# Kernel optimization log

Measured on AMD Instinct MI355X. Metric: run time of the kernel, lower is better.

## Reference

```python
import jax, jax.numpy as jnp
import numpy as np

DIM = 128
NUM_HEADS = 4
HEAD_DIM = DIM // NUM_HEADS
WS = 8            # window size (square)
SHIFT = 4         # shift size
SCALE = HEAD_DIM ** -0.5
WIN_AREA = WS * WS


def _rel_pos_index(wh, ww):
    coords = np.stack(np.meshgrid(np.arange(wh), np.arange(ww), indexing='ij'))  # (2,wh,ww)
    flat = coords.reshape(2, -1)
    rel = flat[:, :, None] - flat[:, None, :]          # (2,S,S)
    rel = rel.transpose(1, 2, 0).astype(np.int64)
    rel[:, :, 0] += wh - 1
    rel[:, :, 1] += ww - 1
    rel[:, :, 0] *= 2 * ww - 1
    return jnp.asarray(rel.sum(-1))                    # (S,S)

_REL_IDX = _rel_pos_index(WS, WS)


def setup_inputs() -> dict:
    key = jax.random.key(0)
    ks = jax.random.split(key, 6)
    B, C, U, V, H, W = 2, DIM, 5, 5, 64, 64
    return {
        'x': jax.random.normal(ks[0], (B, C, U, V, H, W), dtype=jnp.float32),
        'qkv_w': jax.random.normal(ks[1], (3 * DIM, DIM), dtype=jnp.float32) * 0.02,
        'qkv_b': jax.random.normal(ks[2], (3 * DIM,), dtype=jnp.float32) * 0.02,
        'proj_w': jax.random.normal(ks[3], (DIM, DIM), dtype=jnp.float32) * 0.02,
        'proj_b': jax.random.normal(ks[4], (DIM,), dtype=jnp.float32) * 0.02,
        'rpb_table': jax.random.normal(ks[5], ((2 * WS - 1) ** 2, NUM_HEADS), dtype=jnp.float32) * 0.02,
    }


def reference(x, qkv_w, qkv_b, proj_w, proj_b, proj_bias_unused=None, **_):
    # kept signature explicit below; see wrapper
    raise NotImplementedError


def reference(x, qkv_w, qkv_b, proj_w, proj_b, rpb_table):
    B, C, U, V, H, W = x.shape
    Hn, Wn = H // WS, W // WS
    S = WIN_AREA

    # cyclic shift (torch.roll with shifts (SHIFT,SHIFT) on dims (-1,-2))
    xs = jnp.roll(x, (SHIFT, SHIFT), axis=(-1, -2))

    # window partition: B C U V (Hn wv) (Wn wh) -> (B U V Hn Wn) (wv wh) C
    xw = xs.reshape(B, C, U, V, Hn, WS, Wn, WS)
    xw = xw.transpose(0, 2, 3, 4, 6, 5, 7, 1)          # B U V Hn Wn wv wh C
    xw = xw.reshape(-1, S, C)                          # (nW, S, C)

    # qkv projection (torch Linear: x @ W.T + b)
    qkv = xw @ qkv_w.T + qkv_b                         # (nW, S, 3C)
    nW = qkv.shape[0]
    qkv = qkv.reshape(nW, S, NUM_HEADS, 3 * HEAD_DIM).transpose(0, 2, 1, 3)  # (nW,h,S,3d)
    q, k, v = jnp.split(qkv, 3, axis=-1)               # each (nW,h,S,d)

    attn = jnp.einsum('bhqd,bhkd->bhqk', q * SCALE, k)  # (nW,h,S,S)
    bias = rpb_table[_REL_IDX]                          # (S,S,h)
    attn = attn + bias.transpose(2, 0, 1)[None]         # (1,h,S,S) broadcast
    attn = jax.nn.softmax(attn, axis=-1)

    out = jnp.einsum('bhqk,bhkd->bhqd', attn, v)        # (nW,h,S,d)
    out = out.transpose(0, 2, 1, 3).reshape(nW, S, C)   # merge heads
    out = out @ proj_w.T + proj_b

    # window un-partition back to B C U V H W
    out = out.reshape(B, U, V, Hn, Wn, WS, WS, C)
    out = out.transpose(0, 7, 1, 2, 3, 5, 4, 6)         # B C U V Hn wv Wn wh
    out = out.reshape(B, C, U, V, H, W)

    # reverse shift
    return jnp.roll(out, (-SHIFT, -SHIFT), axis=(-1, -2))
```

## Files before the change

### kernel.cpp

```cpp
#include <hip/hip_runtime.h>

#define NH 4
#define HD 32
#define ST 64
#define CD 128
#define IMG 102400
#define VHW 20480
#define HW_ 4096
#define SCALE_ 0.17677669529663687f

typedef __attribute__((ext_vector_type(8))) short bf16x8;
typedef __attribute__((ext_vector_type(4))) float f32x4;
typedef __attribute__((ext_vector_type(4))) int   i32x4;
typedef __attribute__((ext_vector_type(2))) int   i32x2;

__device__ __forceinline__ short f2bf(float f) {
    unsigned int u = __float_as_uint(f);
    u = (u + 0x7FFF + ((u >> 16) & 1)) >> 16;
    return (short)u;
}

__device__ __forceinline__ int cvt_pk_bf16(float lo, float hi) {
    int r;
    asm("v_cvt_pk_bf16_f32 %0, %1, %2" : "=v"(r) : "v"(lo), "v"(hi));
    return r;
}

template <int N>
__device__ __forceinline__ float row_ror(float v) {
    return __int_as_float(__builtin_amdgcn_update_dpp(
        0, __float_as_int(v), 0x120 | N, 0xF, 0xF, true));
}

__global__ void cvt_w_kernel(const float* __restrict__ qkv_w,
                             const float* __restrict__ proj_w,
                             const float* __restrict__ rpb,
                             short* __restrict__ wq,
                             short* __restrict__ wp,
                             float* __restrict__ bt) {
    int i = blockIdx.x * 256 + threadIdx.x;
    if (i < 49152) wq[i] = f2bf(qkv_w[i]);
    else if (i < 65536) wp[i - 49152] = f2bf(proj_w[i - 49152]);
    else if (i < 81920) {
        int j = i - 65536;
        int hh = j >> 12, qi = (j >> 6) & 63, ln2 = (j >> 2) & 15, nt = j & 3;
        int kcol = nt * 16 + ln2;
        int ridx = ((qi >> 3) - (kcol >> 3) + 7) * 15 + ((qi & 7) - (kcol & 7) + 7);
        bt[j] = rpb[ridx * 4 + hh];
    }
}


template <bool DB>
__global__ __launch_bounds__(256, 2)
void win_attn_mfma(const float* __restrict__ x,
                   const short* __restrict__ wq,
                   const float* __restrict__ qkv_b,
                   const short* __restrict__ wp,
                   const float* __restrict__ proj_b,
                   const float* __restrict__ bias,
                   float* __restrict__ out) {
    __shared__ __align__(16) short smem[38400];

    const int t    = threadIdx.x;
    const int h    = __builtin_amdgcn_readfirstlane(t >> 6);
    const int ln   = t & 15;
    const int quad = (t >> 4) & 3;

    const int s     = t & 15;
    const int cb    = t >> 4;
    const int gr    = s >> 1;
    const int ghalf = s & 1;
    const int srow4 = s * 4;

    const int wid = (blockIdx.x & 7) * 400 + (blockIdx.x >> 3);
    const int wn = wid & 7, hn = (wid >> 3) & 7;
    int rem = wid >> 6;
    const int v = rem % 5; rem /= 5;
    const int u = rem % 5;
    const int b = rem / 5;
    const long base = (long)b * (CD * IMG) + u * VHW + v * HW_;

    const int hh_r = (((hn << 3) + gr) - 4) & 63;
    const int ww0  = (((wn << 3) + ghalf * 4) - 4) & 63;
    const long pixrs = base + hh_r * 64 + ww0;

    const int ocol = (((wn << 3) + (quad & 1) * 4) - 4) & 63;

    short* X  = smem;
    short* Qh = smem + 8704 + h * 5120;
    short* Kh = Qh + 2560;
    short* Ph = Qh;
    short* Vh = smem + 29184 + h * 2304;
    short* O  = smem;

    float4 xv[8];
    #pragma unroll
    for (int j = 0; j < 8; ++j)
        xv[j] = *(const float4*)(x + pixrs + (long)(cb * 8 + j) * IMG);

    bf16x8 wqf[24];
    #pragma unroll
    for (int kh = 0; kh < 4; ++kh)
        #pragma unroll
        for (int n = 0; n < 6; ++n)
            wqf[kh * 6 + n] = *(const bf16x8*)(wq + (h * 96 + n * 16 + ln) * 128 + kh * 32 + quad * 8);
    float qb[6];
    #pragma unroll
    for (int n = 0; n < 6; ++n) qb[n] = qkv_b[h * 96 + n * 16 + ln];

    #pragma unroll
    for (int px = 0; px < 4; ++px) {
        i32x4 pk;
        #pragma unroll
        for (int j2 = 0; j2 < 4; ++j2)
            pk[j2] = cvt_pk_bf16(((const float*)&xv[2 * j2])[px],
                                 ((const float*)&xv[2 * j2 + 1])[px]);
        *(i32x4*)(X + (srow4 + px) * 136 + cb * 8) = pk;
    }
    __syncthreads();

    f32x4 acc[6][4];
    #pragma unroll
    for (int n = 0; n < 6; ++n)
        #pragma unroll
        for (int mt = 0; mt < 4; ++mt) acc[n][mt] = (f32x4){0.f, 0.f, 0.f, 0.f};

    #pragma unroll
    for (int kh = 0; kh < 4; ++kh) {
        bf16x8 af[4];
        #pragma unroll
        for (int mt = 0; mt < 4; ++mt)
            af[mt] = *(const bf16x8*)(X + (mt * 16 + ln) * 136 + kh * 32 + quad * 8);
        __builtin_amdgcn_s_setprio(1);
        #pragma unroll
        for (int n = 0; n < 6; ++n)
            #pragma unroll
            for (int mt = 0; mt < 4; ++mt)
                acc[n][mt] = __builtin_amdgcn_mfma_f32_16x16x32_bf16(af[mt], wqf[kh * 6 + n], acc[n][mt], 0, 0, 0);
        __builtin_amdgcn_s_setprio(0);
    }
    __syncthreads();

    #pragma unroll
    for (int n = 0; n < 4; ++n) {
        const float bv_ = qb[n];
        short* dst = (n < 2) ? Qh : Kh;
        const int col = (n & 1) * 16 + ln;
        #pragma unroll
        for (int mt = 0; mt < 4; ++mt)
            #pragma unroll
            for (int r = 0; r < 4; ++r) {
                const float val = acc[n][mt][r] + bv_;
                const int tk = mt * 16 + quad * 4 + r;
                dst[tk * 40 + col] = f2bf((n < 2) ? val * SCALE_ : val);
            }
    }
    #pragma unroll
    for (int n = 4; n < 6; ++n) {
        const float bv_ = qb[n];
        const int d = (n - 4) * 16 + ln;
        #pragma unroll
        for (int mt = 0; mt < 4; ++mt) {
            const int tk0 = mt * 16 + quad * 4;
            i32x2 pv;
            pv[0] = cvt_pk_bf16(acc[n][mt][0] + bv_, acc[n][mt][1] + bv_);
            pv[1] = cvt_pk_bf16(acc[n][mt][2] + bv_, acc[n][mt][3] + bv_);
            *(i32x2*)(Vh + d * 72 + tk0) = pv;
        }
    }

    bf16x8 aq[4], bk[4];
    #pragma unroll
    for (int mt = 0; mt < 4; ++mt) aq[mt] = *(const bf16x8*)(Qh + (mt * 16 + ln) * 40 + quad * 8);
    #pragma unroll
    for (int nt = 0; nt < 4; ++nt) bk[nt] = *(const bf16x8*)(Kh + (nt * 16 + ln) * 40 + quad * 8);

    f32x4 bb[4][4];
    if (DB) {
        const float* bt = bias + h * 4096;
        #pragma unroll
        for (int mt = 0; mt < 4; ++mt)
            #pragma unroll
            for (int r = 0; r < 4; ++r) {
                const int qi = mt * 16 + quad * 4 + r;
                bb[mt][r] = *(const f32x4*)(bt + (qi * 16 + ln) * 4);
            }
    }

    f32x4 sm[4][4];
    __builtin_amdgcn_s_setprio(1);
    #pragma unroll
    for (int mt = 0; mt < 4; ++mt)
        #pragma unroll
        for (int nt = 0; nt < 4; ++nt) {
            f32x4 z = (f32x4){0.f, 0.f, 0.f, 0.f};
            sm[mt][nt] = __builtin_amdgcn_mfma_f32_16x16x32_bf16(aq[mt], bk[nt], z, 0, 0, 0);
        }
    __builtin_amdgcn_s_setprio(0);

    if (DB) {
        #pragma unroll
        for (int mt = 0; mt < 4; ++mt)
            #pragma unroll
            for (int r = 0; r < 4; ++r)
                #pragma unroll
                for (int nt = 0; nt < 4; ++nt)
                    sm[mt][nt][r] += bb[mt][r][nt];
    } else {
        #pragma unroll
        for (int nt = 0; nt < 4; ++nt) {
            const int kcol = nt * 16 + ln;
            const int ik = kcol >> 3, jk = kcol & 7;
            #pragma unroll
            for (int mt = 0; mt < 4; ++mt)
                #pragma unroll
                for (int r = 0; r < 4; ++r) {
                    const int q = mt * 16 + quad * 4 + r;
                    const int ridx = ((q >> 3) - ik + 7) * 15 + ((q & 7) - jk + 7);
                    sm[mt][nt][r] += bias[ridx * 4 + h];
                }
        }
    }

    float inv[4][4];
    #pragma unroll
    for (int mt = 0; mt < 4; ++mt)
        #pragma unroll
        for (int r = 0; r < 4; ++r) {
            float m = fmaxf(fmaxf(sm[mt][0][r], sm[mt][1][r]), fmaxf(sm[mt][2][r], sm[mt][3][r]));
            m = fmaxf(m, row_ror<1>(m));
            m = fmaxf(m, row_ror<2>(m));
            m = fmaxf(m, row_ror<4>(m));
            m = fmaxf(m, row_ror<8>(m));
            float sum = 0.f;
            #pragma unroll
            for (int nt = 0; nt < 4; ++nt) {
                float e = __expf(sm[mt][nt][r] - m);
                sm[mt][nt][r] = e;
                sum += e;
            }
            const int q = mt * 16 + quad * 4 + r;
            #pragma unroll
            for (int nt = 0; nt < 4; ++nt)
                Ph[q * 72 + nt * 16 + ln] = f2bf(sm[mt][nt][r]);
            sum += row_ror<1>(sum);
            sum += row_ror<2>(sum);
            sum += row_ror<4>(sum);
            sum += row_ror<8>(sum);
            inv[mt][r] = 1.f / sum;
        }

    bf16x8 wpf[8];
    #pragma unroll
    for (int kt = 0; kt < 4; ++kt)
        #pragma unroll
        for (int nt = 0; nt < 2; ++nt)
            wpf[kt * 2 + nt] = *(const bf16x8*)(wp + (h * 32 + nt * 16 + ln) * 128 + kt * 32 + quad * 8);
    float pb[2];
    #pragma unroll
    for (int nt = 0; nt < 2; ++nt) pb[nt] = proj_b[h * 32 + nt * 16 + ln];

    f32x4 oa[4][2];
    #pragma unroll
    for (int mt = 0; mt < 4; ++mt)
        #pragma unroll
        for (int nt = 0; nt < 2; ++nt) oa[mt][nt] = (f32x4){0.f, 0.f, 0.f, 0.f};
    #pragma unroll
    for (int kt = 0; kt < 2; ++kt) {
        bf16x8 ap[4], bv[2];
        #pragma unroll
        for (int mt = 0; mt < 4; ++mt)
            ap[mt] = *(const bf16x8*)(Ph + (mt * 16 + ln) * 72 + kt * 32 + quad * 8);
        #pragma unroll
        for (int nt = 0; nt < 2; ++nt)
            bv[nt] = *(const bf16x8*)(Vh + (nt * 16 + ln) * 72 + kt * 32 + quad * 8);
        __builtin_amdgcn_s_setprio(1);
        #pragma unroll
        for (int mt = 0; mt < 4; ++mt)
            #pragma unroll
            for (int nt = 0; nt < 2; ++nt)
                oa[mt][nt] = __builtin_amdgcn_mfma_f32_16x16x32_bf16(ap[mt], bv[nt], oa[mt][nt], 0, 0, 0);
        __builtin_amdgcn_s_setprio(0);
    }

    #pragma unroll
    for (int mt = 0; mt < 4; ++mt)
        #pragma unroll
        for (int nt = 0; nt < 2; ++nt)
            #pragma unroll
            for (int r = 0; r < 4; ++r)
                O[(mt * 16 + quad * 4 + r) * 136 + h * 32 + nt * 16 + ln] =
                    f2bf(oa[mt][nt][r] * inv[mt][r]);
    __syncthreads();

    f32x4 pa[4][2];
    #pragma unroll
    for (int mt = 0; mt < 4; ++mt)
        #pragma unroll
        for (int nt = 0; nt < 2; ++nt) pa[mt][nt] = (f32x4){0.f, 0.f, 0.f, 0.f};
    #pragma unroll
    for (int kt = 0; kt < 4; ++kt) {
        bf16x8 ao[4];
        #pragma unroll
        for (int mt = 0; mt < 4; ++mt)
            ao[mt] = *(const bf16x8*)(O + (mt * 16 + ln) * 136 + kt * 32 + quad * 8);
        __builtin_amdgcn_s_setprio(1);
        #pragma unroll
        for (int mt = 0; mt < 4; ++mt)
            #pragma unroll
            for (int nt = 0; nt < 2; ++nt)
                pa[mt][nt] = __builtin_amdgcn_mfma_f32_16x16x32_bf16(ao[mt], wpf[kt * 2 + nt], pa[mt][nt], 0, 0, 0);
        __builtin_amdgcn_s_setprio(0);
    }

    #pragma unroll
    for (int mt = 0; mt < 4; ++mt) {
        const int orow = (((hn << 3) + 2 * mt + (quad >> 1)) - 4) & 63;
        const long prow = base + orow * 64 + ocol;
        #pragma unroll
        for (int nt = 0; nt < 2; ++nt) {
            const int c = h * 32 + nt * 16 + ln;
            f32x4 fv = pa[mt][nt] + pb[nt];
            *(f32x4*)(out + prow + (long)c * IMG) = fv;
        }
    }
}

__global__ __launch_bounds__(256, 1)
void win_attn_fallback(const float* __restrict__ x,
                       const float* __restrict__ wQKV,
                       const float* __restrict__ qkv_b,
                       const float* __restrict__ wP,
                       const float* __restrict__ proj_b,
                       const float* __restrict__ rpb,
                       float* __restrict__ out) {
    __shared__ __align__(16) float k_lds[NH * ST * HD];
    __shared__ __align__(16) float v_lds[NH * ST * HD];
    const int t = threadIdx.x;
    const int h = __builtin_amdgcn_readfirstlane(t >> 6);
    const int l = t & 63;
    const int wid = blockIdx.x;
    const int wn = wid & 7, hn = (wid >> 3) & 7;
    int rem = wid >> 6;
    const int v = rem % 5; rem /= 5;
    const int u = rem % 5;
    const int b = rem / 5;
    const int hh = (((hn << 3) + (l >> 3)) - 4) & 63;
    const int ww = (((wn << 3) + (l & 7)) - 4) & 63;
    const int pix = b * (NH * HD * IMG) + u * VHW + v * HW_ + hh * 64 + ww;
    float q[HD], kk[HD], vv[HD];
    const float* bq = qkv_b + h * 96;
    #pragma unroll
    for (int d = 0; d < HD; ++d) { q[d] = bq[d]; kk[d] = bq[32 + d]; vv[d] = bq[64 + d]; }
    for (int c = 0; c < CD; ++c) {
        float xv = x[pix + c * IMG];
        const float* wc = wQKV + h * 96 * CD + c;
        #pragma unroll
        for (int d = 0; d < HD; ++d) {
            q[d]  = fmaf(xv, wc[d * CD], q[d]);
            kk[d] = fmaf(xv, wc[(32 + d) * CD], kk[d]);
            vv[d] = fmaf(xv, wc[(64 + d) * CD], vv[d]);
        }
    }
    float* kr = k_lds + (h * ST + l) * HD;
    float* vr = v_lds + (h * ST + l) * HD;
    #pragma unroll
    for (int d = 0; d < HD; ++d) { kr[d] = kk[d]; vr[d] = vv[d]; }
    __syncthreads();
    const float* kh2 = k_lds + h * ST * HD;
    const float* vh2 = v_lds + h * ST * HD;
    const int iq = l >> 3, jq = l & 7;
    float m = -1e30f;
    for (int sk = 0; sk < ST; ++sk) {
        const float* kp = kh2 + sk * HD;
        float a2 = 0.f;
        #pragma unroll
        for (int d = 0; d < HD; ++d) a2 = fmaf(q[d], kp[d], a2);
        int ridx = (iq - (sk >> 3) + 7) * 15 + (jq - (sk & 7) + 7);
        m = fmaxf(m, fmaf(a2, SCALE_, rpb[ridx * 4 + h]));
    }
    float o[HD];
    #pragma unroll
    for (int d = 0; d < HD; ++d) o[d] = 0.f;
    float ssum = 0.f;
    for (int sk = 0; sk < ST; ++sk) {
        const float* kp = kh2 + sk * HD;
        float a2 = 0.f;
        #pragma unroll
        for (int d = 0; d < HD; ++d) a2 = fmaf(q[d], kp[d], a2);
        int ridx = (iq - (sk >> 3) + 7) * 15 + (jq - (sk & 7) + 7);
        float e = __expf(fmaf(a2, SCALE_, rpb[ridx * 4 + h]) - m);
        ssum += e;
        const float* vp = vh2 + sk * HD;
        #pragma unroll
        for (int d = 0; d < HD; ++d) o[d] = fmaf(e, vp[d], o[d]);
    }
    const float inv = 1.f / ssum;
    __syncthreads();
    float* ot = k_lds;
    #pragma unroll
    for (int d = 0; d < HD; ++d) ot[(h * HD + d) * ST + l] = o[d] * inv;
    __syncthreads();
    float o2[HD];
    const float* pb2 = proj_b + h * HD;
    #pragma unroll
    for (int j = 0; j < HD; ++j) o2[j] = pb2[j];
    for (int c = 0; c < CD; ++c) {
        float xv = ot[c * ST + l];
        const float* pc = wP + h * HD * CD + c;
        #pragma unroll
        for (int j = 0; j < HD; ++j) o2[j] = fmaf(xv, pc[j * CD], o2[j]);
    }
    float* ob = out + pix;
    #pragma unroll
    for (int j = 0; j < HD; ++j) ob[(h * HD + j) * IMG] = o2[j];
}

extern "C" void kernel_launch(void* const* d_in, const int* in_sizes, int n_in,
                              void* d_out, int out_size, void* d_ws, size_t ws_size,
                              hipStream_t stream) {
    const float* x      = (const float*)d_in[0];
    const float* qkv_w  = (const float*)d_in[1];
    const float* qkv_b  = (const float*)d_in[2];
    const float* proj_w = (const float*)d_in[3];
    const float* proj_b = (const float*)d_in[4];
    const float* rpb    = (const float*)d_in[5];
    float* out = (float*)d_out;

    const int nW = 2 * 5 * 5 * 8 * 8;
    const size_t need_w  = (size_t)(49152 + 16384) * sizeof(short);
    const size_t need_db = need_w + (size_t)16384 * sizeof(float);

    if (ws_size >= need_db) {
        short* wqs = (short*)d_ws;
        short* wps = wqs + 49152;
        float* bt  = (float*)(wqs + 65536);
        cvt_w_kernel<<<320, 256, 0, stream>>>(qkv_w, proj_w, rpb, wqs, wps, bt);
        win_attn_mfma<true><<<nW, 256, 0, stream>>>(x, wqs, qkv_b, wps, proj_b, bt, out);
    } else if (ws_size >= need_w) {
        short* wqs = (short*)d_ws;
        short* wps = wqs + 49152;
        cvt_w_kernel<<<256, 256, 0, stream>>>(qkv_w, proj_w, rpb, wqs, wps, nullptr);
        win_attn_mfma<false><<<nW, 256, 0, stream>>>(x, wqs, qkv_b, wps, proj_b, rpb, out);
    } else {
        win_attn_fallback<<<nW, 256, 0, stream>>>(x, qkv_w, qkv_b, proj_w, proj_b, rpb, out);
    }
}
```

Baseline: 272.4 us.

## Pack LDS stores via permuted head-dim layout and pre-permuted proj weights

Stores Q/K, P and the attention output to LDS as packed bf16 pairs or quads. To allow this, the head-dim columns and key columns use an interleaved order, which stays consistent because the QK^T and PV contractions are permutation-invariant over the contracted index. The proj weight columns are permuted in the conversion kernel to match the interleaved O layout. The V store changes to scalar stores in permuted token order, and an empty asm forces the wq fragment loads to be issued early. The aim is fewer LDS store instructions and bank conflicts, at the cost of tricky index consistency.

```diff
diff --git a/kernel.cpp b/kernel.cpp
--- a/kernel.cpp
+++ b/kernel.cpp
@@ -40,8 +40,12 @@
                              float* __restrict__ bt) {
     int i = blockIdx.x * 256 + threadIdx.x;
     if (i < 49152) wq[i] = f2bf(qkv_w[i]);
-    else if (i < 65536) wp[i - 49152] = f2bf(proj_w[i - 49152]);
-    else if (i < 81920) {
+    else if (i < 65536) {
+        int j = i - 49152;
+        int oc = j >> 7, cp = j & 127;
+        int src = (cp & 96) | ((cp & 1) << 4) | ((cp & 31) >> 1);
+        wp[j] = f2bf(proj_w[oc * 128 + src]);
+    } else if (i < 81920) {
         int j = i - 65536;
         int hh = j >> 12, qi = (j >> 6) & 63, ln2 = (j >> 2) & 15, nt = j & 3;
         int kcol = nt * 16 + ln2;
@@ -105,6 +109,10 @@
         #pragma unroll
         for (int n = 0; n < 6; ++n)
             wqf[kh * 6 + n] = *(const bf16x8*)(wq + (h * 96 + n * 16 + ln) * 128 + kh * 32 + quad * 8);
+    #pragma unroll
+    for (int i = 0; i < 24; ++i)
+        asm volatile("" :: "v"(wqf[i]));
+
     float qb[6];
     #pragma unroll
     for (int n = 0; n < 6; ++n) qb[n] = qkv_b[h * 96 + n * 16 + ln];
@@ -142,40 +150,6 @@
     }
     __syncthreads();
 
-    #pragma unroll
-    for (int n = 0; n < 4; ++n) {
-        const float bv_ = qb[n];
-        short* dst = (n < 2) ? Qh : Kh;
-        const int col = (n & 1) * 16 + ln;
-        #pragma unroll
-        for (int mt = 0; mt < 4; ++mt)
-            #pragma unroll
-            for (int r = 0; r < 4; ++r) {
-                const float val = acc[n][mt][r] + bv_;
-                const int tk = mt * 16 + quad * 4 + r;
-                dst[tk * 40 + col] = f2bf((n < 2) ? val * SCALE_ : val);
-            }
-    }
-    #pragma unroll
-    for (int n = 4; n < 6; ++n) {
-        const float bv_ = qb[n];
-        const int d = (n - 4) * 16 + ln;
-        #pragma unroll
-        for (int mt = 0; mt < 4; ++mt) {
-            const int tk0 = mt * 16 + quad * 4;
-            i32x2 pv;
-            pv[0] = cvt_pk_bf16(acc[n][mt][0] + bv_, acc[n][mt][1] + bv_);
-            pv[1] = cvt_pk_bf16(acc[n][mt][2] + bv_, acc[n][mt][3] + bv_);
-            *(i32x2*)(Vh + d * 72 + tk0) = pv;
-        }
-    }
-
-    bf16x8 aq[4], bk[4];
-    #pragma unroll
-    for (int mt = 0; mt < 4; ++mt) aq[mt] = *(const bf16x8*)(Qh + (mt * 16 + ln) * 40 + quad * 8);
-    #pragma unroll
-    for (int nt = 0; nt < 4; ++nt) bk[nt] = *(const bf16x8*)(Kh + (nt * 16 + ln) * 40 + quad * 8);
-
     f32x4 bb[4][4];
     if (DB) {
         const float* bt = bias + h * 4096;
@@ -187,6 +161,35 @@
                 bb[mt][r] = *(const f32x4*)(bt + (qi * 16 + ln) * 4);
             }
     }
+
+    #pragma unroll
+    for (int mt = 0; mt < 4; ++mt)
+        #pragma unroll
+        for (int r = 0; r < 4; ++r) {
+            const int tk = mt * 16 + quad * 4 + r;
+            const float q0 = (acc[0][mt][r] + qb[0]) * SCALE_;
+            const float q1 = (acc[1][mt][r] + qb[1]) * SCALE_;
+            *(int*)(Qh + tk * 40 + 2 * ln) = cvt_pk_bf16(q0, q1);
+            const float k0 = acc[2][mt][r] + qb[2];
+            const float k1 = acc[3][mt][r] + qb[3];
+            *(int*)(Kh + tk * 40 + 2 * ln) = cvt_pk_bf16(k0, k1);
+        }
+    #pragma unroll
+    for (int n = 4; n < 6; ++n) {
+        const float bv_ = qb[n];
+        const int d = (n - 4) * 16 + ln;
+        #pragma unroll
+        for (int mt = 0; mt < 4; ++mt)
+            #pragma unroll
+            for (int r = 0; r < 4; ++r)
+                Vh[d * 72 + 16 * quad + 4 * r + mt] = f2bf(acc[n][mt][r] + bv_);
+    }
+
+    bf16x8 aq[4], bk[4];
+    #pragma unroll
+    for (int mt = 0; mt < 4; ++mt) aq[mt] = *(const bf16x8*)(Qh + (mt * 16 + ln) * 40 + quad * 8);
+    #pragma unroll
+    for (int nt = 0; nt < 4; ++nt) bk[nt] = *(const bf16x8*)(Kh + (nt * 16 + ln) * 40 + quad * 8);
 
     f32x4 sm[4][4];
     __builtin_amdgcn_s_setprio(1);
@@ -241,9 +244,10 @@
                 sum += e;
             }
             const int q = mt * 16 + quad * 4 + r;
-            #pragma unroll
-            for (int nt = 0; nt < 4; ++nt)
-                Ph[q * 72 + nt * 16 + ln] = f2bf(sm[mt][nt][r]);
+            i32x2 pv;
+            pv[0] = cvt_pk_bf16(sm[mt][0][r], sm[mt][1][r]);
+            pv[1] = cvt_pk_bf16(sm[mt][2][r], sm[mt][3][r]);
+            *(i32x2*)(Ph + q * 72 + 4 * ln) = pv;
             sum += row_ror<1>(sum);
             sum += row_ror<2>(sum);
             sum += row_ror<4>(sum);
@@ -287,11 +291,11 @@
     #pragma unroll
     for (int mt = 0; mt < 4; ++mt)
         #pragma unroll
-        for (int nt = 0; nt < 2; ++nt)
-            #pragma unroll
-            for (int r = 0; r < 4; ++r)
-                O[(mt * 16 + quad * 4 + r) * 136 + h * 32 + nt * 16 + ln] =
-                    f2bf(oa[mt][nt][r] * inv[mt][r]);
+        for (int r = 0; r < 4; ++r) {
+            const int tok = mt * 16 + quad * 4 + r;
+            *(int*)(O + tok * 136 + h * 32 + 2 * ln) =
+                cvt_pk_bf16(oa[mt][0][r] * inv[mt][r], oa[mt][1][r] * inv[mt][r]);
+        }
     __syncthreads();
 
     f32x4 pa[4][2];
```

Result: no change. 276.5 us (+1.5%).
